# Kernel tuning notes

Measured on AMD Instinct MI355X. Metric: run time of the kernel, lower is better.

The kernel has to match this reference:

```python
import jax, jax.numpy as jnp
import numpy as np

NUM_HEADS = 8

def setup_inputs() -> dict:
    key = jax.random.key(0)
    ks = jax.random.split(key, 9)
    B, C, H, W = 2, 256, 64, 64
    s = 0.02  # weight init scale
    return {
        "x": jax.random.normal(ks[0], (B, C, H, W), dtype=jnp.float32),
        "Wq": jax.random.normal(ks[1], (C, C), dtype=jnp.float32) * s,
        "bq": jnp.zeros((C,), dtype=jnp.float32),
        "Wk": jax.random.normal(ks[2], (C, C), dtype=jnp.float32) * s,
        "bk": jnp.zeros((C,), dtype=jnp.float32),
        "Wv": jax.random.normal(ks[3], (C, C), dtype=jnp.float32) * s,
        "bv": jnp.zeros((C,), dtype=jnp.float32),
        "Wo": jax.random.normal(ks[4], (C, C), dtype=jnp.float32) * s,
        "bo": jnp.zeros((C,), dtype=jnp.float32),
    }

def _conv1x1(x, W, b):
    # 1x1 Conv2d == channel-mixing GEMM: [out_c,in_c] x [B,in_c,H,W]
    return jnp.einsum('oc,bchw->bohw', W, x) + b[None, :, None, None]

def reference(x, Wq, bq, Wk, bk, Wv, bv, Wo, bo):
    B, C, H, W = x.shape
    h = NUM_HEADS
    d = C // h
    N = H * W
    scale = d ** (-0.5)
    q = _conv1x1(x, Wq, bq).reshape(B, h, d, N)
    k = _conv1x1(x, Wk, bk).reshape(B, h, d, N)
    v = _conv1x1(x, Wv, bv).reshape(B, h, d, N)
    attn = jnp.einsum('bhdk,bhdm->bhkm', q, k) * scale  # [B,h,N,N]
    attn = jax.nn.softmax(attn, axis=-1)
    # dropout p=0.0 / eval mode -> identity
    out = jnp.einsum('bhkm,bhdm->bhdk', attn, v)  # [B,h,d,N]
    out = out.reshape(B, C, H, W)
    return x + _conv1x1(out, Wo, bo)
```

## Files before the change

### kernel.cpp

```cpp
#include <hip/hip_runtime.h>

#define B_    2
#define C_    256
#define NH    8
#define HD    32
#define N_    4096
#define SCALE_LOG2E 0.25503485f

typedef float f32x4 __attribute__((ext_vector_type(4)));
typedef short bf16x8 __attribute__((ext_vector_type(8)));

#define MFMA16(a, b, c) __builtin_amdgcn_mfma_f32_16x16x32_bf16(a, b, c, 0, 0, 0)

__device__ __forceinline__ unsigned short f2bf(float f) {
    unsigned int u = __float_as_uint(f);
    u += 0x7fffu + ((u >> 16) & 1u);
    return (unsigned short)(u >> 16);
}

__global__ __launch_bounds__(256) void wconv_kernel(
    const float* __restrict__ Wq, const float* __restrict__ Wk,
    const float* __restrict__ Wv, const float* __restrict__ Wo,
    unsigned short* __restrict__ Wbf)
{
    const int m = blockIdx.y;
    const float* src = (m == 0) ? Wq : (m == 1) ? Wk : (m == 2) ? Wv : Wo;
    const int i = (blockIdx.x * 256 + threadIdx.x) * 4;
    float4 v = *reinterpret_cast<const float4*>(&src[i]);
    unsigned int d0 = (unsigned)f2bf(v.x) | ((unsigned)f2bf(v.y) << 16);
    unsigned int d1 = (unsigned)f2bf(v.z) | ((unsigned)f2bf(v.w) << 16);
    *reinterpret_cast<uint2*>(&Wbf[(size_t)m * 65536 + i]) = make_uint2(d0, d1);
}

__global__ __launch_bounds__(256) void proj_kernel(
    const float* __restrict__ x,
    const unsigned short* __restrict__ Wbf,
    const float* __restrict__ bq, const float* __restrict__ bk,
    const float* __restrict__ bv,
    unsigned short* __restrict__ Qt, unsigned short* __restrict__ Kt,
    unsigned short* __restrict__ Vn)
{
    const int n0 = blockIdx.x * 64;
    const int b  = blockIdx.y;
    const int pr = blockIdx.z;
    const unsigned short* W = Wbf + (size_t)pr * 65536;
    const float* bias = (pr == 0) ? bq : (pr == 1) ? bk : bv;

    __shared__ __align__(16) unsigned short XT[64][264];

    const int t = threadIdx.x;
    #pragma unroll
    for (int s = 0; s < 16; ++s) {
        const int ic = s * 16 + (t >> 4);
        const int nn = (t & 15) * 4;
        float4 v = *reinterpret_cast<const float4*>(&x[((size_t)b * C_ + ic) * N_ + n0 + nn]);
        XT[nn + 0][ic] = f2bf(v.x);
        XT[nn + 1][ic] = f2bf(v.y);
        XT[nn + 2][ic] = f2bf(v.z);
        XT[nn + 3][ic] = f2bf(v.w);
    }
    __syncthreads();

    const int wave = t >> 6, lane = t & 63;
    const int l15 = lane & 15, l4 = lane >> 4;
    const int oc0 = wave * 64;

    f32x4 acc[4][4];
    #pragma unroll
    for (int i = 0; i < 4; ++i)
        #pragma unroll
        for (int j = 0; j < 4; ++j)
            acc[i][j] = (f32x4){0.f, 0.f, 0.f, 0.f};

    #pragma unroll
    for (int kc = 0; kc < 8; ++kc) {
        bf16x8 a[4];
        #pragma unroll
        for (int mi = 0; mi < 4; ++mi)
            a[mi] = *reinterpret_cast<const bf16x8*>(&XT[mi * 16 + l15][kc * 32 + l4 * 8]);
        #pragma unroll
        for (int oci = 0; oci < 4; ++oci) {
            bf16x8 bf = *reinterpret_cast<const bf16x8*>(
                &W[(size_t)(oc0 + oci * 16 + l15) * C_ + kc * 32 + l4 * 8]);
            #pragma unroll
            for (int mi = 0; mi < 4; ++mi)
                acc[mi][oci] = MFMA16(a[mi], bf, acc[mi][oci]);
        }
    }

    const float mult = (pr == 0) ? SCALE_LOG2E : 1.0f;
    #pragma unroll
    for (int oci = 0; oci < 4; ++oci) {
        const int oc = oc0 + oci * 16 + l15;
        const float bb = bias[oc];
        const int h = oc >> 5, d = oc & 31;
        #pragma unroll
        for (int mi = 0; mi < 4; ++mi) {
            #pragma unroll
            for (int r = 0; r < 4; ++r) {
                const int n = n0 + mi * 16 + l4 * 4 + r;
                const unsigned short bfv = f2bf((acc[mi][oci][r] + bb) * mult);
                if (pr == 2)
                    Vn[(((size_t)b * NH + h) * HD + d) * N_ + n] = bfv;
                else if (pr == 0)
                    Qt[(((size_t)b * NH + h) * N_ + n) * HD + d] = bfv;
                else
                    Kt[(((size_t)b * NH + h) * N_ + n) * HD + d] = bfv;
            }
        }
    }
}

__global__ __launch_bounds__(256) void attn_kernel(
    const unsigned short* __restrict__ Qt,
    const unsigned short* __restrict__ Kt,
    const unsigned short* __restrict__ Vn,
    unsigned short* __restrict__ AO)
{
    const int b = blockIdx.z, h = blockIdx.y;
    const int t = threadIdx.x, wave = t >> 6, lane = t & 63;
    const int l15 = lane & 15, l4 = lane >> 4;
    const size_t bh = (size_t)b * NH + h;
    const int qw0 = blockIdx.x * 64 + wave * 16;

    const unsigned short* Qb = Qt + bh * (size_t)N_ * HD;
    const unsigned short* Kb = Kt + bh * (size_t)N_ * HD;
    const unsigned short* Vb = Vn + bh * (size_t)HD * N_;

    __shared__ __align__(16) unsigned short Klds[64][40];
    __shared__ __align__(16) unsigned short Vlds[32][72];
    __shared__ __align__(16) unsigned short Plds[4][16][72];
    unsigned short (*Pw)[72] = Plds[wave];

    const bf16x8 qa = *reinterpret_cast<const bf16x8*>(
        &Qb[(size_t)(qw0 + l15) * HD + l4 * 8]);

    f32x4 o[2];
    o[0] = (f32x4){0.f, 0.f, 0.f, 0.f};
    o[1] = (f32x4){0.f, 0.f, 0.f, 0.f};
    float ls = 0.f;
    const f32x4 zero = (f32x4){0.f, 0.f, 0.f, 0.f};

    for (int kt = 0; kt < N_ / 64; ++kt) {
        {
            const int kr = t >> 2, kcol = (t & 3) * 8;
            *reinterpret_cast<int4*>(&Klds[kr][kcol]) =
                *reinterpret_cast<const int4*>(&Kb[(size_t)(kt * 64 + kr) * HD + kcol]);
            const int vr = t >> 3, vc = (t & 7) * 8;
            *reinterpret_cast<int4*>(&Vlds[vr][vc]) =
                *reinterpret_cast<const int4*>(&Vb[(size_t)vr * N_ + kt * 64 + vc]);
        }
        __syncthreads();

        #pragma unroll
        for (int kf = 0; kf < 4; ++kf) {
            bf16x8 kb = *reinterpret_cast<const bf16x8*>(&Klds[kf * 16 + l15][l4 * 8]);
            f32x4 s = MFMA16(kb, qa, zero);
            float p0 = exp2f(s[0]), p1 = exp2f(s[1]);
            float p2 = exp2f(s[2]), p3 = exp2f(s[3]);
            ls += (p0 + p1) + (p2 + p3);
            unsigned int d0, d1;
            asm("v_cvt_pk_bf16_f32 %0, %1, %2" : "=v"(d0) : "v"(p0), "v"(p1));
            asm("v_cvt_pk_bf16_f32 %0, %1, %2" : "=v"(d1) : "v"(p2), "v"(p3));
            *reinterpret_cast<uint2*>(&Pw[l15][kf * 16 + l4 * 4]) = make_uint2(d0, d1);
        }

        #pragma unroll
        for (int k32 = 0; k32 < 2; ++k32) {
            bf16x8 pa = *reinterpret_cast<const bf16x8*>(&Pw[l15][k32 * 32 + l4 * 8]);
            #pragma unroll
            for (int df = 0; df < 2; ++df) {
                bf16x8 vb = *reinterpret_cast<const bf16x8*>(
                    &Vlds[df * 16 + l15][k32 * 32 + l4 * 8]);
                o[df] = MFMA16(pa, vb, o[df]);
            }
        }
        __syncthreads();
    }

    ls += __shfl_xor(ls, 16, 64);
    ls += __shfl_xor(ls, 32, 64);

    #pragma unroll
    for (int r = 0; r < 4; ++r) {
        const float invr = 1.0f / __shfl(ls, l4 * 4 + r, 64);
        const int q = qw0 + l4 * 4 + r;
        #pragma unroll
        for (int df = 0; df < 2; ++df)
            AO[(bh * (size_t)N_ + q) * HD + df * 16 + l15] = f2bf(o[df][r] * invr);
    }
}

__global__ __launch_bounds__(256) void oproj_kernel(
    const float* __restrict__ x,
    const unsigned short* __restrict__ Wob, const float* __restrict__ bo,
    const unsigned short* __restrict__ AO,
    float* __restrict__ out)
{
    const int b = blockIdx.y;
    const int n0 = blockIdx.x * 32;
    const int t = threadIdx.x, wave = t >> 6, lane = t & 63;
    const int l15 = lane & 15, l4 = lane >> 4;
    const int oc0 = wave * 64;

    f32x4 acc[4][2];
    #pragma unroll
    for (int i = 0; i < 4; ++i)
        #pragma unroll
        for (int j = 0; j < 2; ++j)
            acc[i][j] = (f32x4){0.f, 0.f, 0.f, 0.f};

    #pragma unroll
    for (int kc = 0; kc < 8; ++kc) {
        bf16x8 bfr[2];
        #pragma unroll
        for (int nf = 0; nf < 2; ++nf)
            bfr[nf] = *reinterpret_cast<const bf16x8*>(
                &AO[(((size_t)b * NH + kc) * N_ + n0 + nf * 16 + l15) * HD + l4 * 8]);
        #pragma unroll
        for (int ocf = 0; ocf < 4; ++ocf) {
            bf16x8 a = *reinterpret_cast<const bf16x8*>(
                &Wob[(size_t)(oc0 + ocf * 16 + l15) * C_ + kc * 32 + l4 * 8]);
            #pragma unroll
            for (int nf = 0; nf < 2; ++nf)
                acc[ocf][nf] = MFMA16(a, bfr[nf], acc[ocf][nf]);
        }
    }

    #pragma unroll
    for (int ocf = 0; ocf < 4; ++ocf)
        #pragma unroll
        for (int r = 0; r < 4; ++r) {
            const int oc = oc0 + ocf * 16 + l4 * 4 + r;
            const float bb = bo[oc];
            #pragma unroll
            for (int nf = 0; nf < 2; ++nf) {
                const size_t idx = ((size_t)b * C_ + oc) * (size_t)N_ + n0 + nf * 16 + l15;
                out[idx] = x[idx] + bb + acc[ocf][nf][r];
            }
        }
}

extern "C" void kernel_launch(void* const* d_in, const int* in_sizes, int n_in,
                              void* d_out, int out_size, void* d_ws, size_t ws_size,
                              hipStream_t stream)
{
    const float* x  = (const float*)d_in[0];
    const float* Wq = (const float*)d_in[1];
    const float* bq = (const float*)d_in[2];
    const float* Wk = (const float*)d_in[3];
    const float* bk = (const float*)d_in[4];
    const float* Wv = (const float*)d_in[5];
    const float* bv = (const float*)d_in[6];
    const float* Wo = (const float*)d_in[7];
    const float* bo = (const float*)d_in[8];

    const size_t buf = (size_t)B_ * NH * N_ * HD;
    unsigned short* Qt  = (unsigned short*)d_ws;
    unsigned short* Kt  = Qt + buf;
    unsigned short* Vn  = Kt + buf;
    unsigned short* AO  = Vn + buf;
    unsigned short* Wbf = AO + buf;

    wconv_kernel<<<dim3(64, 4), 256, 0, stream>>>(Wq, Wk, Wv, Wo, Wbf);
    proj_kernel<<<dim3(N_ / 64, B_, 3), 256, 0, stream>>>(
        x, Wbf, bq, bk, bv, Qt, Kt, Vn);
    attn_kernel<<<dim3(N_ / 64, NH, B_), 256, 0, stream>>>(Qt, Kt, Vn, AO);
    oproj_kernel<<<dim3(N_ / 32, B_), 256, 0, stream>>>(
        x, Wbf + 3 * 65536, bo, AO, (float*)d_out);
}
```

Baseline: 216.3 us.

## Use raw exp2, MFMA row sums, and smaller tiles for projection kernels

In the attention loop, libm exp2f is replaced by the hardware v_exp_f32 instruction. The per-lane scalar row-sum accumulation and its final shuffle reduction are replaced by an extra MFMA that multiplies the bf16 probability tile by a ones vector. Separately, the QKV projection and output-projection kernels halve their column tile per block, doubling the grid to raise occupancy and parallelism. The MFMA row sum uses the bf16-rounded probabilities, which keeps the normalizer consistent with the PV product but costs one more MFMA per 32 keys. The smaller tiles reload weights more often.

```diff
diff --git a/kernel.cpp b/kernel.cpp
--- a/kernel.cpp
+++ b/kernel.cpp
@@ -16,6 +16,14 @@
     unsigned int u = __float_as_uint(f);
     u += 0x7fffu + ((u >> 16) & 1u);
     return (unsigned short)(u >> 16);
+}
+
+__device__ __forceinline__ float fast_exp2(float x) {
+#if __has_builtin(__builtin_amdgcn_exp2f)
+    return __builtin_amdgcn_exp2f(x);
+#else
+    float r; asm("v_exp_f32 %0, %1" : "=v"(r) : "v"(x)); return r;
+#endif
 }
 
 __global__ __launch_bounds__(256) void wconv_kernel(
@@ -40,19 +48,19 @@
     unsigned short* __restrict__ Qt, unsigned short* __restrict__ Kt,
     unsigned short* __restrict__ Vn)
 {
-    const int n0 = blockIdx.x * 64;
+    const int n0 = blockIdx.x * 32;
     const int b  = blockIdx.y;
     const int pr = blockIdx.z;
     const unsigned short* W = Wbf + (size_t)pr * 65536;
     const float* bias = (pr == 0) ? bq : (pr == 1) ? bk : bv;
 
-    __shared__ __align__(16) unsigned short XT[64][264];
+    __shared__ __align__(16) unsigned short XT[32][264];
 
     const int t = threadIdx.x;
     #pragma unroll
-    for (int s = 0; s < 16; ++s) {
-        const int ic = s * 16 + (t >> 4);
-        const int nn = (t & 15) * 4;
+    for (int s = 0; s < 8; ++s) {
+        const int ic = s * 32 + (t >> 3);
+        const int nn = (t & 7) * 4;
         float4 v = *reinterpret_cast<const float4*>(&x[((size_t)b * C_ + ic) * N_ + n0 + nn]);
         XT[nn + 0][ic] = f2bf(v.x);
         XT[nn + 1][ic] = f2bf(v.y);
@@ -65,25 +73,25 @@
     const int l15 = lane & 15, l4 = lane >> 4;
     const int oc0 = wave * 64;
 
-    f32x4 acc[4][4];
-    #pragma unroll
-    for (int i = 0; i < 4; ++i)
+    f32x4 acc[2][4];
+    #pragma unroll
+    for (int i = 0; i < 2; ++i)
         #pragma unroll
         for (int j = 0; j < 4; ++j)
             acc[i][j] = (f32x4){0.f, 0.f, 0.f, 0.f};
 
     #pragma unroll
     for (int kc = 0; kc < 8; ++kc) {
-        bf16x8 a[4];
-        #pragma unroll
-        for (int mi = 0; mi < 4; ++mi)
+        bf16x8 a[2];
+        #pragma unroll
+        for (int mi = 0; mi < 2; ++mi)
             a[mi] = *reinterpret_cast<const bf16x8*>(&XT[mi * 16 + l15][kc * 32 + l4 * 8]);
         #pragma unroll
         for (int oci = 0; oci < 4; ++oci) {
             bf16x8 bf = *reinterpret_cast<const bf16x8*>(
                 &W[(size_t)(oc0 + oci * 16 + l15) * C_ + kc * 32 + l4 * 8]);
             #pragma unroll
-            for (int mi = 0; mi < 4; ++mi)
+            for (int mi = 0; mi < 2; ++mi)
                 acc[mi][oci] = MFMA16(a[mi], bf, acc[mi][oci]);
         }
     }
@@ -95,7 +103,7 @@
         const float bb = bias[oc];
         const int h = oc >> 5, d = oc & 31;
         #pragma unroll
-        for (int mi = 0; mi < 4; ++mi) {
+        for (int mi = 0; mi < 2; ++mi) {
             #pragma unroll
             for (int r = 0; r < 4; ++r) {
                 const int n = n0 + mi * 16 + l4 * 4 + r;
@@ -135,10 +143,14 @@
     const bf16x8 qa = *reinterpret_cast<const bf16x8*>(
         &Qb[(size_t)(qw0 + l15) * HD + l4 * 8]);
 
-    f32x4 o[2];
+    bf16x8 ones;
+    #pragma unroll
+    for (int j = 0; j < 8; ++j) ones[j] = (short)0x3F80;
+
+    f32x4 o[2], osum;
     o[0] = (f32x4){0.f, 0.f, 0.f, 0.f};
     o[1] = (f32x4){0.f, 0.f, 0.f, 0.f};
-    float ls = 0.f;
+    osum = (f32x4){0.f, 0.f, 0.f, 0.f};
     const f32x4 zero = (f32x4){0.f, 0.f, 0.f, 0.f};
 
     for (int kt = 0; kt < N_ / 64; ++kt) {
@@ -156,9 +168,8 @@
         for (int kf = 0; kf < 4; ++kf) {
             bf16x8 kb = *reinterpret_cast<const bf16x8*>(&Klds[kf * 16 + l15][l4 * 8]);
             f32x4 s = MFMA16(kb, qa, zero);
-            float p0 = exp2f(s[0]), p1 = exp2f(s[1]);
-            float p2 = exp2f(s[2]), p3 = exp2f(s[3]);
-            ls += (p0 + p1) + (p2 + p3);
+            float p0 = fast_exp2(s[0]), p1 = fast_exp2(s[1]);
+            float p2 = fast_exp2(s[2]), p3 = fast_exp2(s[3]);
             unsigned int d0, d1;
             asm("v_cvt_pk_bf16_f32 %0, %1, %2" : "=v"(d0) : "v"(p0), "v"(p1));
             asm("v_cvt_pk_bf16_f32 %0, %1, %2" : "=v"(d1) : "v"(p2), "v"(p3));
@@ -168,6 +179,7 @@
         #pragma unroll
         for (int k32 = 0; k32 < 2; ++k32) {
             bf16x8 pa = *reinterpret_cast<const bf16x8*>(&Pw[l15][k32 * 32 + l4 * 8]);
+            osum = MFMA16(pa, ones, osum);
             #pragma unroll
             for (int df = 0; df < 2; ++df) {
                 bf16x8 vb = *reinterpret_cast<const bf16x8*>(
@@ -178,12 +190,9 @@
         __syncthreads();
     }
 
-    ls += __shfl_xor(ls, 16, 64);
-    ls += __shfl_xor(ls, 32, 64);
-
     #pragma unroll
     for (int r = 0; r < 4; ++r) {
-        const float invr = 1.0f / __shfl(ls, l4 * 4 + r, 64);
+        const float invr = 1.0f / osum[r];
         const int q = qw0 + l4 * 4 + r;
         #pragma unroll
         for (int df = 0; df < 2; ++df)
@@ -198,32 +207,25 @@
     float* __restrict__ out)
 {
     const int b = blockIdx.y;
-    const int n0 = blockIdx.x * 32;
+    const int n0 = blockIdx.x * 16;
     const int t = threadIdx.x, wave = t >> 6, lane = t & 63;
     const int l15 = lane & 15, l4 = lane >> 4;
     const int oc0 = wave * 64;
 
-    f32x4 acc[4][2];
+    f32x4 acc[4];
     #pragma unroll
     for (int i = 0; i < 4; ++i)
-        #pragma unroll
-        for (int j = 0; j < 2; ++j)
-            acc[i][j] = (f32x4){0.f, 0.f, 0.f, 0.f};
+        acc[i] = (f32x4){0.f, 0.f, 0.f, 0.f};
 
     #pragma unroll
     for (int kc = 0; kc < 8; ++kc) {
-        bf16x8 bfr[2];
-        #pragma unroll
-        for (int nf = 0; nf < 2; ++nf)
-            bfr[nf] = *reinterpret_cast<const bf16x8*>(
-                &AO[(((size_t)b * NH + kc) * N_ + n0 + nf * 16 + l15) * HD + l4 * 8]);
+        bf16x8 bfr = *reinterpret_cast<const bf16x8*>(
+            &AO[(((size_t)b * NH + kc) * N_ + n0 + l15) * HD + l4 * 8]);
         #pragma unroll
         for (int ocf = 0; ocf < 4; ++ocf) {
             bf16x8 a = *reinterpret_cast<const bf16x8*>(
                 &Wob[(size_t)(oc0 + ocf * 16 + l15) * C_ + kc * 32 + l4 * 8]);
-            #pragma unroll
-            for (int nf = 0; nf < 2; ++nf)
-                acc[ocf][nf] = MFMA16(a, bfr[nf], acc[ocf][nf]);
+            acc[ocf] = MFMA16(a, bfr, acc[ocf]);
         }
     }
 
@@ -232,12 +234,8 @@
         #pragma unroll
         for (int r = 0; r < 4; ++r) {
             const int oc = oc0 + ocf * 16 + l4 * 4 + r;
-            const float bb = bo[oc];
-            #pragma unroll
-            for (int nf = 0; nf < 2; ++nf) {
-                const size_t idx = ((size_t)b * C_ + oc) * (size_t)N_ + n0 + nf * 16 + l15;
-                out[idx] = x[idx] + bb + acc[ocf][nf][r];
-            }
+            const size_t idx = ((size_t)b * C_ + oc) * (size_t)N_ + n0 + l15;
+            out[idx] = x[idx] + bo[oc] + acc[ocf][r];
         }
 }
 
@@ -263,9 +261,9 @@
     unsigned short* Wbf = AO + buf;
 
     wconv_kernel<<<dim3(64, 4), 256, 0, stream>>>(Wq, Wk, Wv, Wo, Wbf);
-    proj_kernel<<<dim3(N_ / 64, B_, 3), 256, 0, stream>>>(
+    proj_kernel<<<dim3(N_ / 32, B_, 3), 256, 0, stream>>>(
         x, Wbf, bq, bk, bv, Qt, Kt, Vn);
     attn_kernel<<<dim3(N_ / 64, NH, B_), 256, 0, stream>>>(Qt, Kt, Vn, AO);
-    oproj_kernel<<<dim3(N_ / 32, B_), 256, 0, stream>>>(
+    oproj_kernel<<<dim3(N_ / 16, B_), 256, 0, stream>>>(
         x, Wbf + 3 * 65536, bo, AO, (float*)d_out);
 }
```

Result: faster. 201.9 us (-6.7%).
